# Kernel optimization log

Hardware: AMD Instinct MI355X
Metric: run time of the kernel (lower is better)

Reference implementation:

```python
import jax, jax.numpy as jnp
import numpy as np
from jax import lax

K = 16      # neighbors per point (module init arg)
B = 16      # number of point clouds (equal-sized, per batch ids)
P = 4096    # points per cloud


def setup_inputs() -> dict:
    key = jax.random.key(0)
    x = jax.random.normal(key, (B * P, 3), dtype=jnp.float32)
    batch = jnp.repeat(jnp.arange(B, dtype=jnp.int64), P)  # sorted, equal-sized clouds
    return {"x": x, "batch": batch}


def _knn_indices(xb):
    # xb: (B, P, 3). Squared pairwise distances via |a|^2 + |b|^2 - 2 a.b
    sq = jnp.sum(xb * xb, axis=-1)                      # (B, P)
    d = sq[:, :, None] + sq[:, None, :] - 2.0 * jnp.einsum('bpc,bqc->bpq', xb, xb)
    # knn_graph(loop=False): exclude self-edges
    eye = jnp.eye(P, dtype=bool)
    d = jnp.where(eye[None], jnp.inf, d)                # (B, P, P)
    _, idx = lax.top_k(-d, K)                            # (B, P, K) nearest neighbors
    return idx


def reference(x, batch):
    # batch ids are sorted with equal cloud sizes -> dense per-cloud layout
    xb = x.reshape(B, P, 3)
    idx = _knn_indices(xb)                               # (B, P, K)
    neighbors = jax.vmap(lambda pts, ind: pts[ind])(xb, idx)  # (B, P, K, 3)
    mean = neighbors.mean(axis=2, keepdims=True)         # (B, P, 1, 3)
    c = neighbors - mean
    cov = jnp.einsum('bpki,bpkj->bpij', c, c) / K        # (B, P, 3, 3)
    out = jnp.concatenate([xb, cov.reshape(B, P, 9)], axis=-1)
    return out.reshape(B * P, 12)
```

## Files before the change

### kernel.cpp

```cpp
#include <hip/hip_runtime.h>

#define PTS    4096
#define TPB    256
#define PPB    64
#define QTR    1024
#define QPR    512
#define CAP    36
#define NCLOUD 16
#define NPAIRS (NCLOUD * PTS / 2)
#define UMAX   0xFFFFFFFFu

typedef __attribute__((ext_vector_type(2))) float f32x2;

template<int N>
__device__ __forceinline__ void insN(unsigned key, unsigned (&s)[N], unsigned &cmax) {
  if (key < cmax) {
    bool done = false;
#pragma unroll
    for (int i = 0; i < N; ++i) {
      bool c = (!done) && (s[i] == cmax);
      s[i] = c ? key : s[i];
      done = done || c;
    }
    cmax = s[0];
#pragma unroll
    for (int i = 1; i < N; ++i) cmax = (s[i] > cmax) ? s[i] : cmax;
  }
}

__global__ void pair_pack(const float* __restrict__ x, float* __restrict__ ws) {
  const int g = blockIdx.x * TPB + threadIdx.x;
  const float* s = x + (size_t)g * 6;
  const float2 f01 = *(const float2*)(s + 0);
  const float2 f23 = *(const float2*)(s + 2);
  const float2 f45 = *(const float2*)(s + 4);
  float* d = ws + (size_t)g * 8;
  *(float4*)(d)     = make_float4(f01.x, f23.y, f01.y, f45.x);
  *(float2*)(d + 4) = make_float2(f23.x, f45.y);
}

__global__ __launch_bounds__(TPB, 4) void knn_cov_pk(const float* __restrict__ ws,
                                                     float* __restrict__ out) {
  __shared__ unsigned scol[CAP * TPB];
  __shared__ unsigned scnt[TPB];

  const int tid  = threadIdx.x;
  const int lane = tid & 63;
  const int h     = __builtin_amdgcn_readfirstlane(tid >> 6);
  const int cloud = blockIdx.x >> 6;
  const int chunk = blockIdx.x & 63;
  const int p     = chunk * PPB + lane;

  const float* __restrict__ wc = ws + (size_t)cloud * (PTS / 2) * 8;

  const float* mp = wc + (size_t)(p >> 1) * 8;
  const int pe = p & 1;
  const float px = mp[0 + pe], py = mp[2 + pe], pz = mp[4 + pe];
  f32x2 vx; vx.x = px; vx.y = px;
  f32x2 vy; vy.x = py; vy.y = py;
  f32x2 vz; vz.x = pz; vz.y = pz;

  const int c0 = h * QTR;
  const float* __restrict__ cp = wc + (size_t)(c0 >> 1) * 8;

  f32x2 m2[32];
#pragma unroll
  for (int j = 0; j < 32; ++j) { m2[j].x = 3.4e38f; m2[j].y = 3.4e38f; }
  for (int t0 = 0; t0 < QPR; t0 += 32) {
#pragma unroll
    for (int g = 0; g < 8; ++g) {
#pragma unroll
      for (int j = 0; j < 4; ++j) {
        const int pi = t0 + g * 4 + j;
        const float4 a  = *(const float4*)(cp + (size_t)pi * 8);
        const f32x2  zz = *(const f32x2*)(cp + (size_t)pi * 8 + 4);
        f32x2 xs; xs.x = a.x; xs.y = a.y;
        f32x2 ys; ys.x = a.z; ys.y = a.w;
        const f32x2 dx = xs - vx, dy = ys - vy, dz = zz - vz;
        const f32x2 d  = dx * dx + dy * dy + dz * dz;
        const int mi   = g * 4 + j;
        m2[mi] = __builtin_elementwise_min(m2[mi], d);
      }
    }
  }

  float mm[64];
#pragma unroll
  for (int j = 0; j < 32; ++j) { mm[2 * j] = m2[j].x; mm[2 * j + 1] = m2[j].y; }
  unsigned s17[17], cm;
#pragma unroll
  for (int j = 0; j < 17; ++j) s17[j] = __float_as_uint(mm[j]);
  cm = s17[0];
#pragma unroll
  for (int j = 1; j < 17; ++j) cm = (s17[j] > cm) ? s17[j] : cm;
#pragma unroll
  for (int j = 17; j < 64; ++j) insN<17>(__float_as_uint(mm[j]), s17, cm);
  const float Tval = __uint_as_float(cm);

  unsigned cnt = 0;
  for (int t0 = 0; t0 < QPR; t0 += 8) {
#pragma unroll
    for (int j = 0; j < 8; ++j) {
      const int pi = t0 + j;
      const float4 a  = *(const float4*)(cp + (size_t)pi * 8);
      const f32x2  zz = *(const f32x2*)(cp + (size_t)pi * 8 + 4);
      f32x2 xs; xs.x = a.x; xs.y = a.y;
      f32x2 ys; ys.x = a.z; ys.y = a.w;
      const f32x2 dx = xs - vx, dy = ys - vy, dz = zz - vz;
      const f32x2 d  = dx * dx + dy * dy + dz * dz;
      if (d.x <= Tval) {
        const unsigned slot = (cnt < (unsigned)CAP) ? cnt : (unsigned)(CAP - 1);
        scol[slot * TPB + tid] =
            (__float_as_uint(d.x) & 0xFFFFF000u) | (unsigned)(c0 + 2 * pi);
        cnt++;
      }
      if (d.y <= Tval) {
        const unsigned slot = (cnt < (unsigned)CAP) ? cnt : (unsigned)(CAP - 1);
        scol[slot * TPB + tid] =
            (__float_as_uint(d.y) & 0xFFFFF000u) | (unsigned)(c0 + 2 * pi + 1);
        cnt++;
      }
    }
  }

  if (cnt > (unsigned)CAP) {
    unsigned sf[17], cmf = UMAX;
#pragma unroll
    for (int j = 0; j < 17; ++j) sf[j] = UMAX;
    for (int ci = 0; ci < QTR; ++ci) {
      const float* q = cp + (size_t)(ci >> 1) * 8;
      const int e = ci & 1;
      const float dx = q[0 + e] - px, dy = q[2 + e] - py, dz = q[4 + e] - pz;
      const float d  = fmaf(dz, dz, fmaf(dy, dy, dx * dx));
      insN<17>((__float_as_uint(d) & 0xFFFFF000u) | (unsigned)(c0 + ci), sf, cmf);
    }
#pragma unroll
    for (int j = 0; j < 17; ++j) scol[j * TPB + tid] = sf[j];
    cnt = 17;
  }
  scnt[tid] = cnt;
  __syncthreads();

  if (tid < PPB) {
    unsigned s16[16], cm16 = UMAX;
#pragma unroll
    for (int j = 0; j < 16; ++j) s16[j] = UMAX;
    const unsigned selfk = (unsigned)p;
#pragma unroll
    for (int k = 0; k < 4; ++k) {
      const int col = k * PPB + tid;
      const unsigned n = scnt[col];
      unsigned w = n;
#pragma unroll
      for (int off = 32; off >= 1; off >>= 1) {
        unsigned o = (unsigned)__shfl_xor((int)w, off, 64);
        w = (o > w) ? o : w;
      }
      for (unsigned j = 0; j < w; ++j) {
        unsigned kb = (j < n) ? scol[j * TPB + col] : UMAX;
        kb = (kb == selfk) ? UMAX : kb;
        insN<16>(kb, s16, cm16);
      }
    }

    float Sx = 0, Sy = 0, Sz = 0;
    float Sxx = 0, Sxy = 0, Sxz = 0, Syy = 0, Syz = 0, Szz = 0;
#pragma unroll
    for (int j = 0; j < 16; ++j) {
      const int idx = (int)(s16[j] & 0xFFFu);
      const float* q = wc + (size_t)(idx >> 1) * 8;
      const int e = idx & 1;
      const float nx = q[0 + e], ny = q[2 + e], nz = q[4 + e];
      Sx += nx; Sy += ny; Sz += nz;
      Sxx = fmaf(nx, nx, Sxx); Sxy = fmaf(nx, ny, Sxy); Sxz = fmaf(nx, nz, Sxz);
      Syy = fmaf(ny, ny, Syy); Syz = fmaf(ny, nz, Syz); Szz = fmaf(nz, nz, Szz);
    }
    const float sc = 0.0625f;
    const float mx = Sx * sc, my = Sy * sc, mz = Sz * sc;
    const float cxx = fmaf(-mx, mx, Sxx * sc);
    const float cxy = fmaf(-mx, my, Sxy * sc);
    const float cxz = fmaf(-mx, mz, Sxz * sc);
    const float cyy = fmaf(-my, my, Syy * sc);
    const float cyz = fmaf(-my, mz, Syz * sc);
    const float czz = fmaf(-mz, mz, Szz * sc);

    const int gid = cloud * PTS + p;
    float4* o4 = (float4*)(out + (size_t)gid * 12);
    o4[0] = make_float4(px, py, pz, cxx);
    o4[1] = make_float4(cxy, cxz, cxy, cyy);
    o4[2] = make_float4(cyz, cxz, cyz, czz);
  }
}

__global__ __launch_bounds__(TPB, 4) void knn_cov_aos(const float* __restrict__ x,
                                                      float* __restrict__ out) {
  __shared__ unsigned scol[CAP * TPB];
  __shared__ unsigned scnt[TPB];

  const int tid  = threadIdx.x;
  const int lane = tid & 63;
  const int h     = __builtin_amdgcn_readfirstlane(tid >> 6);
  const int cloud = blockIdx.x >> 6;
  const int chunk = blockIdx.x & 63;
  const int p     = chunk * PPB + lane;

  const float* __restrict__ xc = x + (size_t)cloud * PTS * 3;
  const float px = xc[p * 3 + 0], py = xc[p * 3 + 1], pz = xc[p * 3 + 2];
  const int c0 = h * QTR;
  const float* __restrict__ cc = xc + (size_t)c0 * 3;

  float m[64];
#pragma unroll
  for (int j = 0; j < 64; ++j) m[j] = 3.4e38f;
  for (int t0 = 0; t0 < QTR; t0 += 64) {
#pragma unroll
    for (int g = 0; g < 8; ++g) {
#pragma unroll
      for (int j = 0; j < 8; ++j) {
        const int ci = t0 + g * 8 + j;
        const float dx = cc[ci * 3 + 0] - px, dy = cc[ci * 3 + 1] - py,
                    dz = cc[ci * 3 + 2] - pz;
        const float d = fmaf(dz, dz, fmaf(dy, dy, dx * dx));
        const int mi = g * 8 + j;
        m[mi] = fminf(m[mi], d);
      }
    }
  }
  unsigned s17[17], cm;
#pragma unroll
  for (int j = 0; j < 17; ++j) s17[j] = __float_as_uint(m[j]);
  cm = s17[0];
#pragma unroll
  for (int j = 1; j < 17; ++j) cm = (s17[j] > cm) ? s17[j] : cm;
#pragma unroll
  for (int j = 17; j < 64; ++j) insN<17>(__float_as_uint(m[j]), s17, cm);
  const float Tval = __uint_as_float(cm);

  unsigned cnt = 0;
  for (int t0 = 0; t0 < QTR; t0 += 8) {
#pragma unroll
    for (int j = 0; j < 8; ++j) {
      const int ci = t0 + j;
      const float dx = cc[ci * 3 + 0] - px, dy = cc[ci * 3 + 1] - py,
                  dz = cc[ci * 3 + 2] - pz;
      const float d = fmaf(dz, dz, fmaf(dy, dy, dx * dx));
      if (d <= Tval) {
        const unsigned slot = (cnt < (unsigned)CAP) ? cnt : (unsigned)(CAP - 1);
        scol[slot * TPB + tid] =
            (__float_as_uint(d) & 0xFFFFF000u) | (unsigned)(c0 + ci);
        cnt++;
      }
    }
  }
  if (cnt > (unsigned)CAP) {
    unsigned sf[17], cmf = UMAX;
#pragma unroll
    for (int j = 0; j < 17; ++j) sf[j] = UMAX;
    for (int ci = 0; ci < QTR; ++ci) {
      const float dx = cc[ci * 3 + 0] - px, dy = cc[ci * 3 + 1] - py,
                  dz = cc[ci * 3 + 2] - pz;
      const float d = fmaf(dz, dz, fmaf(dy, dy, dx * dx));
      insN<17>((__float_as_uint(d) & 0xFFFFF000u) | (unsigned)(c0 + ci), sf, cmf);
    }
#pragma unroll
    for (int j = 0; j < 17; ++j) scol[j * TPB + tid] = sf[j];
    cnt = 17;
  }
  scnt[tid] = cnt;
  __syncthreads();

  if (tid < PPB) {
    unsigned s16[16], cm16 = UMAX;
#pragma unroll
    for (int j = 0; j < 16; ++j) s16[j] = UMAX;
    const unsigned selfk = (unsigned)p;
#pragma unroll
    for (int k = 0; k < 4; ++k) {
      const int col = k * PPB + tid;
      const unsigned n = scnt[col];
      unsigned w = n;
#pragma unroll
      for (int off = 32; off >= 1; off >>= 1) {
        unsigned o = (unsigned)__shfl_xor((int)w, off, 64);
        w = (o > w) ? o : w;
      }
      for (unsigned j = 0; j < w; ++j) {
        unsigned kb = (j < n) ? scol[j * TPB + col] : UMAX;
        kb = (kb == selfk) ? UMAX : kb;
        insN<16>(kb, s16, cm16);
      }
    }
    float Sx = 0, Sy = 0, Sz = 0;
    float Sxx = 0, Sxy = 0, Sxz = 0, Syy = 0, Syz = 0, Szz = 0;
#pragma unroll
    for (int j = 0; j < 16; ++j) {
      const int idx = (int)(s16[j] & 0xFFFu);
      const float nx = xc[idx * 3 + 0], ny = xc[idx * 3 + 1], nz = xc[idx * 3 + 2];
      Sx += nx; Sy += ny; Sz += nz;
      Sxx = fmaf(nx, nx, Sxx); Sxy = fmaf(nx, ny, Sxy); Sxz = fmaf(nx, nz, Sxz);
      Syy = fmaf(ny, ny, Syy); Syz = fmaf(ny, nz, Syz); Szz = fmaf(nz, nz, Szz);
    }
    const float sc = 0.0625f;
    const float mx = Sx * sc, my = Sy * sc, mz = Sz * sc;
    const float cxx = fmaf(-mx, mx, Sxx * sc);
    const float cxy = fmaf(-mx, my, Sxy * sc);
    const float cxz = fmaf(-mx, mz, Sxz * sc);
    const float cyy = fmaf(-my, my, Syy * sc);
    const float cyz = fmaf(-my, mz, Syz * sc);
    const float czz = fmaf(-mz, mz, Szz * sc);

    const int gid = cloud * PTS + p;
    float4* o4 = (float4*)(out + (size_t)gid * 12);
    o4[0] = make_float4(px, py, pz, cxx);
    o4[1] = make_float4(cxy, cxz, cxy, cyy);
    o4[2] = make_float4(cyz, cxz, cyz, czz);
  }
}

extern "C" void kernel_launch(void* const* d_in, const int* in_sizes, int n_in,
                              void* d_out, int out_size, void* d_ws, size_t ws_size,
                              hipStream_t stream) {
  const float* x = (const float*)d_in[0];
  float* out = (float*)d_out;
  dim3 grid(NCLOUD * (PTS / PPB));
  if (ws_size >= (size_t)NPAIRS * 8 * sizeof(float)) {
    float* ws = (float*)d_ws;
    pair_pack<<<NPAIRS / TPB, TPB, 0, stream>>>(x, ws);
    knn_cov_pk<<<grid, TPB, 0, stream>>>(ws, out);
  } else {
    knn_cov_aos<<<grid, TPB, 0, stream>>>(x, out);
  }
}
```

Baseline: 215.5 us.

## Split candidates into 8 segments with shared cross-segment threshold and quad SoA packing

Repacks points into 4-point SoA quads so each candidate load is three float4s. The fast kernel now handles 32 query points per block, with 8 segments of 512 candidates each instead of 4 of 1024. The per-segment 17-smallest bucket minima are merged in shared memory into one global threshold per query, so the filter pass keeps far fewer candidates and the buffer capacity drops to 17. This costs extra barriers and a serial merge on 32 threads, and it raises the occupancy hint to 6.

```diff
diff --git a/kernel.cpp b/kernel.cpp
--- a/kernel.cpp
+++ b/kernel.cpp
@@ -2,12 +2,12 @@
 
 #define PTS    4096
 #define TPB    256
-#define PPB    64
-#define QTR    1024
-#define QPR    512
-#define CAP    36
+#define PPB    32
+#define NSEG   8
+#define SEG    512
+#define CAP    17
 #define NCLOUD 16
-#define NPAIRS (NCLOUD * PTS / 2)
+#define NQUADS (NCLOUD * PTS / 4)
 #define UMAX   0xFFFFFFFFu
 
 typedef __attribute__((ext_vector_type(2))) float f32x2;
@@ -28,96 +28,144 @@
   }
 }
 
-__global__ void pair_pack(const float* __restrict__ x, float* __restrict__ ws) {
+__global__ void quad_pack(const float* __restrict__ x, float* __restrict__ ws) {
   const int g = blockIdx.x * TPB + threadIdx.x;
-  const float* s = x + (size_t)g * 6;
-  const float2 f01 = *(const float2*)(s + 0);
-  const float2 f23 = *(const float2*)(s + 2);
-  const float2 f45 = *(const float2*)(s + 4);
-  float* d = ws + (size_t)g * 8;
-  *(float4*)(d)     = make_float4(f01.x, f23.y, f01.y, f45.x);
-  *(float2*)(d + 4) = make_float2(f23.x, f45.y);
-}
-
-__global__ __launch_bounds__(TPB, 4) void knn_cov_pk(const float* __restrict__ ws,
-                                                     float* __restrict__ out) {
-  __shared__ unsigned scol[CAP * TPB];
+  const float* s = x + (size_t)g * 12;
+  const float4 a = *(const float4*)(s + 0);
+  const float4 b = *(const float4*)(s + 4);
+  const float4 c = *(const float4*)(s + 8);
+  float* d = ws + (size_t)g * 12;
+  *(float4*)(d + 0) = make_float4(a.x, a.w, b.z, c.y);
+  *(float4*)(d + 4) = make_float4(a.y, b.x, b.w, c.z);
+  *(float4*)(d + 8) = make_float4(a.z, b.y, c.x, c.w);
+}
+
+__global__ __launch_bounds__(TPB, 6) void knn_cov_q(const float* __restrict__ ws,
+                                                    float* __restrict__ out) {
+  __shared__ unsigned sbuf[CAP * TPB];
   __shared__ unsigned scnt[TPB];
-
-  const int tid  = threadIdx.x;
-  const int lane = tid & 63;
-  const int h     = __builtin_amdgcn_readfirstlane(tid >> 6);
-  const int cloud = blockIdx.x >> 6;
-  const int chunk = blockIdx.x & 63;
-  const int p     = chunk * PPB + lane;
-
-  const float* __restrict__ wc = ws + (size_t)cloud * (PTS / 2) * 8;
-
-  const float* mp = wc + (size_t)(p >> 1) * 8;
-  const int pe = p & 1;
-  const float px = mp[0 + pe], py = mp[2 + pe], pz = mp[4 + pe];
+  __shared__ unsigned sT[PPB];
+
+  const int tid   = threadIdx.x;
+  const int pt    = tid & (PPB - 1);
+  const int seg   = tid >> 5;
+  const int cloud = blockIdx.x >> 7;
+  const int chunk = blockIdx.x & 127;
+  const int p     = chunk * PPB + pt;
+
+  const float* __restrict__ wc = ws + (size_t)cloud * (PTS / 4) * 12;
+
+  const float* mp = wc + (size_t)(p >> 2) * 12;
+  const int pe = p & 3;
+  const float px = mp[0 + pe], py = mp[4 + pe], pz = mp[8 + pe];
   f32x2 vx; vx.x = px; vx.y = px;
   f32x2 vy; vy.x = py; vy.y = py;
   f32x2 vz; vz.x = pz; vz.y = pz;
 
-  const int c0 = h * QTR;
-  const float* __restrict__ cp = wc + (size_t)(c0 >> 1) * 8;
-
-  f32x2 m2[32];
-#pragma unroll
-  for (int j = 0; j < 32; ++j) { m2[j].x = 3.4e38f; m2[j].y = 3.4e38f; }
-  for (int t0 = 0; t0 < QPR; t0 += 32) {
-#pragma unroll
-    for (int g = 0; g < 8; ++g) {
-#pragma unroll
-      for (int j = 0; j < 4; ++j) {
-        const int pi = t0 + g * 4 + j;
-        const float4 a  = *(const float4*)(cp + (size_t)pi * 8);
-        const f32x2  zz = *(const f32x2*)(cp + (size_t)pi * 8 + 4);
-        f32x2 xs; xs.x = a.x; xs.y = a.y;
-        f32x2 ys; ys.x = a.z; ys.y = a.w;
-        const f32x2 dx = xs - vx, dy = ys - vy, dz = zz - vz;
-        const f32x2 d  = dx * dx + dy * dy + dz * dz;
-        const int mi   = g * 4 + j;
-        m2[mi] = __builtin_elementwise_min(m2[mi], d);
-      }
-    }
-  }
-
-  float mm[64];
-#pragma unroll
-  for (int j = 0; j < 32; ++j) { mm[2 * j] = m2[j].x; mm[2 * j + 1] = m2[j].y; }
+  const int c0 = seg * SEG;
+  const float* __restrict__ cp = wc + (size_t)(c0 >> 2) * 12;
+
+  f32x2 m2[16];
+#pragma unroll
+  for (int j = 0; j < 16; ++j) { m2[j].x = 3.4e38f; m2[j].y = 3.4e38f; }
+#pragma unroll 1
+  for (int t0 = 0; t0 < SEG / 4; t0 += 8) {
+#pragma unroll
+    for (int q = 0; q < 8; ++q) {
+      const float* qb = cp + (size_t)(t0 + q) * 12;
+      const float4 X = *(const float4*)(qb + 0);
+      const float4 Y = *(const float4*)(qb + 4);
+      const float4 Z = *(const float4*)(qb + 8);
+      f32x2 x01; x01.x = X.x; x01.y = X.y;
+      f32x2 x23; x23.x = X.z; x23.y = X.w;
+      f32x2 y01; y01.x = Y.x; y01.y = Y.y;
+      f32x2 y23; y23.x = Y.z; y23.y = Y.w;
+      f32x2 z01; z01.x = Z.x; z01.y = Z.y;
+      f32x2 z23; z23.x = Z.z; z23.y = Z.w;
+      const f32x2 dx0 = x01 - vx, dy0 = y01 - vy, dz0 = z01 - vz;
+      const f32x2 dx1 = x23 - vx, dy1 = y23 - vy, dz1 = z23 - vz;
+      const f32x2 d01 = dx0 * dx0 + dy0 * dy0 + dz0 * dz0;
+      const f32x2 d23 = dx1 * dx1 + dy1 * dy1 + dz1 * dz1;
+      m2[2 * q]     = __builtin_elementwise_min(m2[2 * q], d01);
+      m2[2 * q + 1] = __builtin_elementwise_min(m2[2 * q + 1], d23);
+    }
+  }
+
+  unsigned mm[32];
+#pragma unroll
+  for (int j = 0; j < 16; ++j) {
+    mm[2 * j]     = __float_as_uint(m2[j].x);
+    mm[2 * j + 1] = __float_as_uint(m2[j].y);
+  }
   unsigned s17[17], cm;
 #pragma unroll
-  for (int j = 0; j < 17; ++j) s17[j] = __float_as_uint(mm[j]);
+  for (int j = 0; j < 17; ++j) s17[j] = mm[j];
   cm = s17[0];
 #pragma unroll
   for (int j = 1; j < 17; ++j) cm = (s17[j] > cm) ? s17[j] : cm;
 #pragma unroll
-  for (int j = 17; j < 64; ++j) insN<17>(__float_as_uint(mm[j]), s17, cm);
-  const float Tval = __uint_as_float(cm);
+  for (int j = 17; j < 32; ++j) insN<17>(mm[j], s17, cm);
+
+#pragma unroll
+  for (int j = 0; j < 17; ++j) sbuf[j * TPB + tid] = s17[j];
+  __syncthreads();
+  if (tid < PPB) {
+    unsigned t17[17], cmt;
+#pragma unroll
+    for (int j = 0; j < 17; ++j) t17[j] = sbuf[j * TPB + tid];
+    cmt = t17[0];
+#pragma unroll
+    for (int j = 1; j < 17; ++j) cmt = (t17[j] > cmt) ? t17[j] : cmt;
+#pragma unroll 1
+    for (int sg = 1; sg < NSEG; ++sg) {
+      const int col = sg * PPB + tid;
+#pragma unroll
+      for (int j = 0; j < 17; ++j) insN<17>(sbuf[j * TPB + col], t17, cmt);
+    }
+    sT[tid] = cmt;
+  }
+  __syncthreads();
+  const float Tval = __uint_as_float(sT[pt]);
+  __syncthreads();
 
   unsigned cnt = 0;
-  for (int t0 = 0; t0 < QPR; t0 += 8) {
-#pragma unroll
-    for (int j = 0; j < 8; ++j) {
-      const int pi = t0 + j;
-      const float4 a  = *(const float4*)(cp + (size_t)pi * 8);
-      const f32x2  zz = *(const f32x2*)(cp + (size_t)pi * 8 + 4);
-      f32x2 xs; xs.x = a.x; xs.y = a.y;
-      f32x2 ys; ys.x = a.z; ys.y = a.w;
-      const f32x2 dx = xs - vx, dy = ys - vy, dz = zz - vz;
-      const f32x2 d  = dx * dx + dy * dy + dz * dz;
-      if (d.x <= Tval) {
+#pragma unroll 1
+  for (int t0 = 0; t0 < SEG / 4; t0 += 8) {
+#pragma unroll
+    for (int q = 0; q < 8; ++q) {
+      const float* qb = cp + (size_t)(t0 + q) * 12;
+      const float4 X = *(const float4*)(qb + 0);
+      const float4 Y = *(const float4*)(qb + 4);
+      const float4 Z = *(const float4*)(qb + 8);
+      f32x2 x01; x01.x = X.x; x01.y = X.y;
+      f32x2 x23; x23.x = X.z; x23.y = X.w;
+      f32x2 y01; y01.x = Y.x; y01.y = Y.y;
+      f32x2 y23; y23.x = Y.z; y23.y = Y.w;
+      f32x2 z01; z01.x = Z.x; z01.y = Z.y;
+      f32x2 z23; z23.x = Z.z; z23.y = Z.w;
+      const f32x2 dx0 = x01 - vx, dy0 = y01 - vy, dz0 = z01 - vz;
+      const f32x2 dx1 = x23 - vx, dy1 = y23 - vy, dz1 = z23 - vz;
+      const f32x2 d01 = dx0 * dx0 + dy0 * dy0 + dz0 * dz0;
+      const f32x2 d23 = dx1 * dx1 + dy1 * dy1 + dz1 * dz1;
+      const unsigned ib = (unsigned)(c0 + 4 * (t0 + q));
+      if (d01.x <= Tval) {
         const unsigned slot = (cnt < (unsigned)CAP) ? cnt : (unsigned)(CAP - 1);
-        scol[slot * TPB + tid] =
-            (__float_as_uint(d.x) & 0xFFFFF000u) | (unsigned)(c0 + 2 * pi);
-        cnt++;
-      }
-      if (d.y <= Tval) {
+        sbuf[slot * TPB + tid] = (__float_as_uint(d01.x) & 0xFFFFF000u) | ib;
+        cnt++;
+      }
+      if (d01.y <= Tval) {
         const unsigned slot = (cnt < (unsigned)CAP) ? cnt : (unsigned)(CAP - 1);
-        scol[slot * TPB + tid] =
-            (__float_as_uint(d.y) & 0xFFFFF000u) | (unsigned)(c0 + 2 * pi + 1);
+        sbuf[slot * TPB + tid] = (__float_as_uint(d01.y) & 0xFFFFF000u) | (ib + 1);
+        cnt++;
+      }
+      if (d23.x <= Tval) {
+        const unsigned slot = (cnt < (unsigned)CAP) ? cnt : (unsigned)(CAP - 1);
+        sbuf[slot * TPB + tid] = (__float_as_uint(d23.x) & 0xFFFFF000u) | (ib + 2);
+        cnt++;
+      }
+      if (d23.y <= Tval) {
+        const unsigned slot = (cnt < (unsigned)CAP) ? cnt : (unsigned)(CAP - 1);
+        sbuf[slot * TPB + tid] = (__float_as_uint(d23.y) & 0xFFFFF000u) | (ib + 3);
         cnt++;
       }
     }
@@ -127,37 +175,33 @@
     unsigned sf[17], cmf = UMAX;
 #pragma unroll
     for (int j = 0; j < 17; ++j) sf[j] = UMAX;
-    for (int ci = 0; ci < QTR; ++ci) {
-      const float* q = cp + (size_t)(ci >> 1) * 8;
-      const int e = ci & 1;
-      const float dx = q[0 + e] - px, dy = q[2 + e] - py, dz = q[4 + e] - pz;
+#pragma unroll 1
+    for (int ci = 0; ci < SEG; ++ci) {
+      const float* qb = cp + (size_t)(ci >> 2) * 12;
+      const int e = ci & 3;
+      const float dx = qb[e] - px, dy = qb[4 + e] - py, dz = qb[8 + e] - pz;
       const float d  = fmaf(dz, dz, fmaf(dy, dy, dx * dx));
       insN<17>((__float_as_uint(d) & 0xFFFFF000u) | (unsigned)(c0 + ci), sf, cmf);
     }
 #pragma unroll
-    for (int j = 0; j < 17; ++j) scol[j * TPB + tid] = sf[j];
+    for (int j = 0; j < 17; ++j) sbuf[j * TPB + tid] = sf[j];
     cnt = 17;
   }
-  scnt[tid] = cnt;
+  scnt[tid] = (cnt < (unsigned)CAP) ? cnt : (unsigned)CAP;
   __syncthreads();
 
   if (tid < PPB) {
+    const int pm = chunk * PPB + tid;
     unsigned s16[16], cm16 = UMAX;
 #pragma unroll
     for (int j = 0; j < 16; ++j) s16[j] = UMAX;
-    const unsigned selfk = (unsigned)p;
-#pragma unroll
-    for (int k = 0; k < 4; ++k) {
-      const int col = k * PPB + tid;
+    const unsigned selfk = (unsigned)pm;
+#pragma unroll 1
+    for (int sg = 0; sg < NSEG; ++sg) {
+      const int col = sg * PPB + tid;
       const unsigned n = scnt[col];
-      unsigned w = n;
-#pragma unroll
-      for (int off = 32; off >= 1; off >>= 1) {
-        unsigned o = (unsigned)__shfl_xor((int)w, off, 64);
-        w = (o > w) ? o : w;
-      }
-      for (unsigned j = 0; j < w; ++j) {
-        unsigned kb = (j < n) ? scol[j * TPB + col] : UMAX;
+      for (unsigned j = 0; j < n; ++j) {
+        unsigned kb = sbuf[j * TPB + col];
         kb = (kb == selfk) ? UMAX : kb;
         insN<16>(kb, s16, cm16);
       }
@@ -168,9 +212,9 @@
 #pragma unroll
     for (int j = 0; j < 16; ++j) {
       const int idx = (int)(s16[j] & 0xFFFu);
-      const float* q = wc + (size_t)(idx >> 1) * 8;
-      const int e = idx & 1;
-      const float nx = q[0 + e], ny = q[2 + e], nz = q[4 + e];
+      const float* qb = wc + (size_t)(idx >> 2) * 12;
+      const int e = idx & 3;
+      const float nx = qb[e], ny = qb[4 + e], nz = qb[8 + e];
       Sx += nx; Sy += ny; Sz += nz;
       Sxx = fmaf(nx, nx, Sxx); Sxy = fmaf(nx, ny, Sxy); Sxz = fmaf(nx, nz, Sxz);
       Syy = fmaf(ny, ny, Syy); Syz = fmaf(ny, nz, Syz); Szz = fmaf(nz, nz, Szz);
@@ -184,17 +228,22 @@
     const float cyz = fmaf(-my, mz, Syz * sc);
     const float czz = fmaf(-mz, mz, Szz * sc);
 
-    const int gid = cloud * PTS + p;
+    const int gid = cloud * PTS + pm;
+    const float ox = wc[(size_t)(pm >> 2) * 12 + (pm & 3)];
+    const float oy = wc[(size_t)(pm >> 2) * 12 + 4 + (pm & 3)];
+    const float oz = wc[(size_t)(pm >> 2) * 12 + 8 + (pm & 3)];
     float4* o4 = (float4*)(out + (size_t)gid * 12);
-    o4[0] = make_float4(px, py, pz, cxx);
+    o4[0] = make_float4(ox, oy, oz, cxx);
     o4[1] = make_float4(cxy, cxz, cxy, cyy);
     o4[2] = make_float4(cyz, cxz, cyz, czz);
   }
 }
 
+#define QTRF   1024
+#define CAPF   36
 __global__ __launch_bounds__(TPB, 4) void knn_cov_aos(const float* __restrict__ x,
                                                       float* __restrict__ out) {
-  __shared__ unsigned scol[CAP * TPB];
+  __shared__ unsigned scol[CAPF * TPB];
   __shared__ unsigned scnt[TPB];
 
   const int tid  = threadIdx.x;
@@ -202,17 +251,17 @@
   const int h     = __builtin_amdgcn_readfirstlane(tid >> 6);
   const int cloud = blockIdx.x >> 6;
   const int chunk = blockIdx.x & 63;
-  const int p     = chunk * PPB + lane;
+  const int p     = chunk * 64 + lane;
 
   const float* __restrict__ xc = x + (size_t)cloud * PTS * 3;
   const float px = xc[p * 3 + 0], py = xc[p * 3 + 1], pz = xc[p * 3 + 2];
-  const int c0 = h * QTR;
+  const int c0 = h * QTRF;
   const float* __restrict__ cc = xc + (size_t)c0 * 3;
 
   float m[64];
 #pragma unroll
   for (int j = 0; j < 64; ++j) m[j] = 3.4e38f;
-  for (int t0 = 0; t0 < QTR; t0 += 64) {
+  for (int t0 = 0; t0 < QTRF; t0 += 64) {
 #pragma unroll
     for (int g = 0; g < 8; ++g) {
 #pragma unroll
@@ -237,7 +286,7 @@
   const float Tval = __uint_as_float(cm);
 
   unsigned cnt = 0;
-  for (int t0 = 0; t0 < QTR; t0 += 8) {
+  for (int t0 = 0; t0 < QTRF; t0 += 8) {
 #pragma unroll
     for (int j = 0; j < 8; ++j) {
       const int ci = t0 + j;
@@ -245,18 +294,18 @@
                   dz = cc[ci * 3 + 2] - pz;
       const float d = fmaf(dz, dz, fmaf(dy, dy, dx * dx));
       if (d <= Tval) {
-        const unsigned slot = (cnt < (unsigned)CAP) ? cnt : (unsigned)(CAP - 1);
+        const unsigned slot = (cnt < (unsigned)CAPF) ? cnt : (unsigned)(CAPF - 1);
         scol[slot * TPB + tid] =
             (__float_as_uint(d) & 0xFFFFF000u) | (unsigned)(c0 + ci);
         cnt++;
       }
     }
   }
-  if (cnt > (unsigned)CAP) {
+  if (cnt > (unsigned)CAPF) {
     unsigned sf[17], cmf = UMAX;
 #pragma unroll
     for (int j = 0; j < 17; ++j) sf[j] = UMAX;
-    for (int ci = 0; ci < QTR; ++ci) {
+    for (int ci = 0; ci < QTRF; ++ci) {
       const float dx = cc[ci * 3 + 0] - px, dy = cc[ci * 3 + 1] - py,
                   dz = cc[ci * 3 + 2] - pz;
       const float d = fmaf(dz, dz, fmaf(dy, dy, dx * dx));
@@ -269,23 +318,17 @@
   scnt[tid] = cnt;
   __syncthreads();
 
-  if (tid < PPB) {
+  if (tid < 64) {
     unsigned s16[16], cm16 = UMAX;
 #pragma unroll
     for (int j = 0; j < 16; ++j) s16[j] = UMAX;
     const unsigned selfk = (unsigned)p;
 #pragma unroll
     for (int k = 0; k < 4; ++k) {
-      const int col = k * PPB + tid;
+      const int col = k * 64 + tid;
       const unsigned n = scnt[col];
-      unsigned w = n;
-#pragma unroll
-      for (int off = 32; off >= 1; off >>= 1) {
-        unsigned o = (unsigned)__shfl_xor((int)w, off, 64);
-        w = (o > w) ? o : w;
-      }
-      for (unsigned j = 0; j < w; ++j) {
-        unsigned kb = (j < n) ? scol[j * TPB + col] : UMAX;
+      for (unsigned j = 0; j < n; ++j) {
+        unsigned kb = scol[j * TPB + col];
         kb = (kb == selfk) ? UMAX : kb;
         insN<16>(kb, s16, cm16);
       }
@@ -322,12 +365,11 @@
                               hipStream_t stream) {
   const float* x = (const float*)d_in[0];
   float* out = (float*)d_out;
-  dim3 grid(NCLOUD * (PTS / PPB));
-  if (ws_size >= (size_t)NPAIRS * 8 * sizeof(float)) {
+  if (ws_size >= (size_t)NQUADS * 12 * sizeof(float)) {
     float* ws = (float*)d_ws;
-    pair_pack<<<NPAIRS / TPB, TPB, 0, stream>>>(x, ws);
-    knn_cov_pk<<<grid, TPB, 0, stream>>>(ws, out);
+    quad_pack<<<NQUADS / TPB, TPB, 0, stream>>>(x, ws);
+    knn_cov_q<<<dim3(NCLOUD * (PTS / PPB)), TPB, 0, stream>>>(ws, out);
   } else {
-    knn_cov_aos<<<grid, TPB, 0, stream>>>(x, out);
-  }
-}
+    knn_cov_aos<<<dim3(NCLOUD * 64), TPB, 0, stream>>>(x, out);
+  }
+}
```

Measured after the change: 273.9 us. +27.1%, slower.
